# Performance work log

Measured on AMD Instinct MI355X. Metric: run time of the kernel, lower is better.

Reference implementation:

```python
import jax, jax.numpy as jnp
import numpy as np

B, L, D, V, S, R = 4096, 128, 100, 800000, 1024, 512
EPS = 1e-5

def setup_inputs() -> dict:
    key = jax.random.key(0)
    ks = jax.random.split(key, 10)
    bound = float(np.sqrt(6.0 / D))
    return {
        "statement_vecs": jax.random.normal(ks[0], (B, S), jnp.float32),
        "qa_ids": jax.random.randint(ks[1], (B, L, 2), 0, V),
        "qa_lens": jax.random.randint(ks[2], (B,), 0, L + 1),
        "emb": jax.random.uniform(ks[3], (V, D), jnp.float32, -bound, bound),
        "W1": jax.random.normal(ks[4], (2 * D + S, 2 * R), jnp.float32) * 0.02,
        "b1": jnp.zeros((2 * R,), jnp.float32),
        "g1": jnp.ones((2 * R,), jnp.float32),
        "beta1": jnp.zeros((2 * R,), jnp.float32),
        "W2": jax.random.normal(ks[5], (2 * R, R), jnp.float32) * 0.02,
        "b2": jnp.zeros((R,), jnp.float32),
        "g2": jnp.ones((R,), jnp.float32),
        "beta2": jnp.zeros((R,), jnp.float32),
        "W3": jax.random.normal(ks[6], (R, 1), jnp.float32) * 0.02,
        "b3": jnp.zeros((1,), jnp.float32),
    }

def _batchnorm(x, g, b):
    # BatchNorm1d in training mode: biased batch statistics over batch dim
    m = x.mean(0)
    v = ((x - m) ** 2).mean(0)
    return (x - m) * jax.lax.rsqrt(v + EPS) * g + b

def reference(statement_vecs, qa_ids, qa_lens, emb, W1, b1, g1, beta1, W2, b2, g2, beta2, W3, b3):
    # ragged mean-pool of (L_i, 2, D) concept embeddings, zero vector if length 0
    mask = (jnp.arange(L)[None, :] < qa_lens[:, None]).astype(emb.dtype)  # [B, L]
    qa_embed = emb[qa_ids]                                                # [B, L, 2, D]
    denom = jnp.maximum(qa_lens, 1).astype(emb.dtype)                     # avoid /0 (sum is 0 then)
    qa_pooled = (qa_embed * mask[:, :, None, None]).sum(1) / denom[:, None, None]  # [B, 2, D]
    qa_pooled = qa_pooled.reshape(B, 2 * D)
    qas = jnp.concatenate([qa_pooled, statement_vecs], axis=1)            # [B, 2D+S]
    # relation_extractor: Linear -> ReLU -> BN -> Linear -> BN -> ReLU
    h = _batchnorm(jax.nn.relu(qas @ W1 + b1), g1, beta1)
    h = jax.nn.relu(_batchnorm(h @ W2 + b2, g2, beta2))
    logits = h @ W3 + b3                                                  # [B, 1]
    return logits
```

## Files before the change

kernel.cpp:

```cpp
#include <hip/hip_runtime.h>
#include <hip/hip_bf16.h>

#define B_ 4096
#define L_ 128
#define D_ 100
#define S_ 1024
#define R_ 512
#define K1P_ 1280
#define N1_ 1024
#define EPS_ 1e-5f

typedef short bf16x8 __attribute__((ext_vector_type(8)));
typedef short short4v __attribute__((ext_vector_type(4)));
typedef float f32x4 __attribute__((ext_vector_type(4)));

static __device__ __forceinline__ short f2bf(float x) {
  union { float f; unsigned u; } c; c.f = x;
  unsigned r = (c.u + 0x7fffu + ((c.u >> 16) & 1u)) >> 16;
  return (short)r;
}
static __device__ __forceinline__ float bf2f(short x) {
  union { unsigned u; float f; } c; c.u = ((unsigned)(unsigned short)x) << 16;
  return c.f;
}

__global__ __launch_bounds__(256) void prep_kernel(
    const float* __restrict__ sv, const int* __restrict__ qa_ids,
    const int* __restrict__ qa_lens, const float* __restrict__ emb,
    const float* __restrict__ W1, short* __restrict__ qas,
    short* __restrict__ W1t) {
  int t = threadIdx.x;
  if (blockIdx.x < B_) {
    int b = blockIdx.x;
    __shared__ int ids[L_ * 2];
    __shared__ __align__(16) float partial[4][D_];
    int len = qa_lens[b];
    ids[t] = qa_ids[(size_t)b * (L_ * 2) + t];
    __syncthreads();
    int w = t >> 6, l = t & 63;
    if (l < 25) {
      float4 a = {0.f, 0.f, 0.f, 0.f};
      for (int r = w; r < 2 * len; r += 4) {
        const float* row = emb + (size_t)ids[r] * D_;
        float4 v = *reinterpret_cast<const float4*>(row + l * 4);
        a.x += v.x; a.y += v.y; a.z += v.z; a.w += v.w;
      }
      *reinterpret_cast<float4*>(&partial[w][l * 4]) = a;
    }
    __syncthreads();
    short* qrow = qas + (size_t)b * K1P_;
    if (t < 200) {
      int k = t / 100, d = t - k * 100;
      float s = partial[k][d] + partial[k + 2][d];
      qrow[t] = f2bf(s / (float)(len > 0 ? len : 1));
    }
    {
      float4 v = *reinterpret_cast<const float4*>(sv + (size_t)b * S_ + t * 4);
      short4v o;
      o[0] = f2bf(v.x); o[1] = f2bf(v.y); o[2] = f2bf(v.z); o[3] = f2bf(v.w);
      *(short4v*)&qrow[200 + t * 4] = o;
    }
    if (t < K1P_ - 1224) qrow[1224 + t] = 0;
  } else {
    __shared__ float tile[32][33];
    int bx = blockIdx.x - B_;
    int n0 = (bx & 31) * 32, k0 = (bx >> 5) * 32;
#pragma unroll
    for (int p = 0; p < 4; ++p) {
      int kk = (t >> 5) + p * 8, nn = t & 31;
      int k = k0 + kk;
      tile[kk][nn] = (k < 1224) ? W1[(size_t)k * N1_ + n0 + nn] : 0.f;
    }
    __syncthreads();
#pragma unroll
    for (int p = 0; p < 4; ++p) {
      int nn = (t >> 5) + p * 8, kk = t & 31;
      W1t[(size_t)(n0 + nn) * K1P_ + k0 + kk] = f2bf(tile[kk][nn]);
    }
  }
}

template <int ROWS>
static __device__ __forceinline__ void stage_tile64(
    const short* __restrict__ gp, int stride, int k0, short* lds, int t) {
#pragma unroll
  for (int p = 0; p < ROWS / 32; ++p) {
    int off16 = p * 256 + t;
    int r = off16 >> 3;
    int c = off16 & 7;
    int kc = c ^ (r & 7);
    const short* g = gp + (size_t)r * stride + k0 + kc * 8;
    __builtin_amdgcn_global_load_lds(
        (const __attribute__((address_space(1))) void*)g,
        (__attribute__((address_space(3))) void*)(lds + (size_t)off16 * 8),
        16, 0, 0);
  }
}

template <int BM, int BN, int WM, int WN, bool RELU, int NBIAS>
__global__ __launch_bounds__(256) void mfma_gemm(
    const short* __restrict__ A, const short* __restrict__ Bt,
    const float* __restrict__ biasp, short* __restrict__ C,
    float* __restrict__ part, int K, int N) {
  constexpr int FM = BM / WM / 16;
  constexpr int FN = BN / WN / 16;
  __shared__ short As[2][BM * 64];
  __shared__ short Bs[2][BN * 64];
  __shared__ float sred[WM][WN][FN][16];
  __shared__ float qred[WM][WN][FN][16];
  const int t = threadIdx.x;
  const int l = t & 63, w = t >> 6;
  const int wr = w / WN, wc = w % WN;
  const int row0 = blockIdx.y * BM, col0 = blockIdx.x * BN;
  const short* Ab = A + (size_t)row0 * K;
  const short* Bb = Bt + (size_t)col0 * K;
  f32x4 acc[FM][FN] = {};
  const int lrow = l & 15, lkc = l >> 4;
  const int nt = K / 64;
  stage_tile64<BM>(Ab, K, 0, As[0], t);
  stage_tile64<BN>(Bb, K, 0, Bs[0], t);
  __syncthreads();
  for (int ts = 0; ts < nt; ++ts) {
    const int cur = ts & 1;
    if (ts + 1 < nt) {
      stage_tile64<BM>(Ab, K, (ts + 1) * 64, As[cur ^ 1], t);
      stage_tile64<BN>(Bb, K, (ts + 1) * 64, Bs[cur ^ 1], t);
    }
    bf16x8 af[2][FM], bfr[2][FN];
#pragma unroll
    for (int ks = 0; ks < 2; ++ks) {
#pragma unroll
      for (int m = 0; m < FM; ++m) {
        int r = wr * (BM / WM) + m * 16 + lrow;
        int ch = (ks * 4 + lkc) ^ (r & 7);
        af[ks][m] = *(const bf16x8*)&As[cur][r * 64 + ch * 8];
      }
#pragma unroll
      for (int n = 0; n < FN; ++n) {
        int r = wc * (BN / WN) + n * 16 + lrow;
        int ch = (ks * 4 + lkc) ^ (r & 7);
        bfr[ks][n] = *(const bf16x8*)&Bs[cur][r * 64 + ch * 8];
      }
    }
#pragma unroll
    for (int ks = 0; ks < 2; ++ks)
#pragma unroll
      for (int m = 0; m < FM; ++m)
#pragma unroll
        for (int n = 0; n < FN; ++n)
          acc[m][n] = __builtin_amdgcn_mfma_f32_16x16x32_bf16(
              af[ks][m], bfr[ks][n], acc[m][n], 0, 0, 0);
    __syncthreads();
  }
  float ss[FN], qq[FN];
#pragma unroll
  for (int n = 0; n < FN; ++n) { ss[n] = 0.f; qq[n] = 0.f; }
#pragma unroll
  for (int m = 0; m < FM; ++m) {
#pragma unroll
    for (int n = 0; n < FN; ++n) {
      int col = col0 + wc * (BN / WN) + n * 16 + lrow;
      float bv = 0.f;
#pragma unroll
      for (int i = 0; i < NBIAS; ++i) bv += biasp[(size_t)i * N + col];
#pragma unroll
      for (int j = 0; j < 4; ++j) {
        int row = row0 + wr * (BM / WM) + m * 16 + (l >> 4) * 4 + j;
        float v = acc[m][n][j] + bv;
        if (RELU) v = fmaxf(v, 0.f);
        short vb = f2bf(v);
        C[(size_t)row * N + col] = vb;
        float f = bf2f(vb);
        ss[n] += f;
        qq[n] += f * f;
      }
    }
  }
#pragma unroll
  for (int n = 0; n < FN; ++n) {
    ss[n] += __shfl_xor(ss[n], 16);
    ss[n] += __shfl_xor(ss[n], 32);
    qq[n] += __shfl_xor(qq[n], 16);
    qq[n] += __shfl_xor(qq[n], 32);
  }
  if (l < 16) {
#pragma unroll
    for (int n = 0; n < FN; ++n) {
      sred[wr][wc][n][l] = ss[n];
      qred[wr][wc][n][l] = qq[n];
    }
  }
  __syncthreads();
  if (t < WN * FN * 16) {
    int c16 = t & 15, n = (t >> 4) % FN, wcc = t / (16 * FN);
    float s = 0.f, q = 0.f;
#pragma unroll
    for (int r = 0; r < WM; ++r) { s += sred[r][wcc][n][c16]; q += qred[r][wcc][n][c16]; }
    int col = col0 + wcc * (BN / WN) + n * 16 + c16;
    part[(size_t)blockIdx.y * 2 * N + col] = s;
    part[(size_t)blockIdx.y * 2 * N + N + col] = q;
  }
}

__global__ __launch_bounds__(256) void fold_tile(
    const float* __restrict__ part1, const float* __restrict__ W2,
    const float* __restrict__ b2, const float* __restrict__ g1,
    const float* __restrict__ beta1, short* __restrict__ W2pt,
    float* __restrict__ pbias) {
  int kt = blockIdx.x, jt = blockIdx.y;
  int t = threadIdx.x;
  int k0 = kt * 64, j0 = jt * 64;
  __shared__ float a1s[64], c1s[64];
  __shared__ float tT[64][65];
  __shared__ float bred[16][64];
  if (t < 64) {
    float s = 0.f, q = 0.f;
    for (int b = 0; b < 32; ++b) {
      s += part1[(size_t)b * 2048 + k0 + t];
      q += part1[(size_t)b * 2048 + 1024 + k0 + t];
    }
    float mean = s * (1.f / B_);
    float var = q * (1.f / B_) - mean * mean;
    float a = g1[k0 + t] * rsqrtf(var + EPS_);
    a1s[t] = a;
    c1s[t] = beta1[k0 + t] - mean * a;
  }
  __syncthreads();
  int g = t >> 4, j4 = t & 15;
  float pb0 = 0.f, pb1 = 0.f, pb2 = 0.f, pb3 = 0.f;
#pragma unroll
  for (int p = 0; p < 4; ++p) {
    int kk = g + p * 16;
    float4 wv = *(const float4*)&W2[(size_t)(k0 + kk) * R_ + j0 + j4 * 4];
    float a = a1s[kk], cc = c1s[kk];
    tT[j4 * 4 + 0][kk] = a * wv.x;
    tT[j4 * 4 + 1][kk] = a * wv.y;
    tT[j4 * 4 + 2][kk] = a * wv.z;
    tT[j4 * 4 + 3][kk] = a * wv.w;
    pb0 += cc * wv.x; pb1 += cc * wv.y; pb2 += cc * wv.z; pb3 += cc * wv.w;
  }
  bred[g][j4 * 4 + 0] = pb0;
  bred[g][j4 * 4 + 1] = pb1;
  bred[g][j4 * 4 + 2] = pb2;
  bred[g][j4 * 4 + 3] = pb3;
  __syncthreads();
#pragma unroll
  for (int p = 0; p < 4; ++p) {
    int jj = g + p * 16;
    short4v o;
    o[0] = f2bf(tT[jj][j4 * 4 + 0]);
    o[1] = f2bf(tT[jj][j4 * 4 + 1]);
    o[2] = f2bf(tT[jj][j4 * 4 + 2]);
    o[3] = f2bf(tT[jj][j4 * 4 + 3]);
    *(short4v*)&W2pt[(size_t)(j0 + jj) * N1_ + k0 + j4 * 4] = o;
  }
  if (t < 64) {
    float pbv = 0.f;
#pragma unroll
    for (int gg = 0; gg < 16; ++gg) pbv += bred[gg][t];
    if (kt == 0) pbv += b2[j0 + t];
    pbias[(size_t)kt * R_ + j0 + t] = pbv;
  }
}

__global__ __launch_bounds__(256) void reduce_bn2(
    const float* __restrict__ part2, const float* __restrict__ g2,
    const float* __restrict__ beta2, float* __restrict__ a2c2) {
  int j = blockIdx.x * 256 + threadIdx.x;
  if (j >= R_) return;
  float s = 0.f, q = 0.f;
  for (int b = 0; b < 64; ++b) {
    s += part2[(size_t)b * 1024 + j];
    q += part2[(size_t)b * 1024 + 512 + j];
  }
  float mean = s * (1.f / B_);
  float var = q * (1.f / B_) - mean * mean;
  float a = g2[j] * rsqrtf(var + EPS_);
  a2c2[j] = a;
  a2c2[R_ + j] = beta2[j] - mean * a;
}

__global__ __launch_bounds__(256) void final_kernel(
    const short* __restrict__ z2, const float* __restrict__ a2c2,
    const float* __restrict__ W3, const float* __restrict__ b3,
    float* __restrict__ out) {
  int wave = threadIdx.x >> 6;
  int lane = threadIdx.x & 63;
  int row = blockIdx.x * 4 + wave;
  const short* zr = z2 + (size_t)row * R_;
  int j0 = lane * 8;
  bf16x8 zv = *(const bf16x8*)&zr[j0];
  float acc = 0.f;
#pragma unroll
  for (int i = 0; i < 8; ++i) {
    float h = fmaxf(bf2f(zv[i]) * a2c2[j0 + i] + a2c2[R_ + j0 + i], 0.f);
    acc += h * W3[j0 + i];
  }
  for (int off = 32; off > 0; off >>= 1) acc += __shfl_down(acc, off, 64);
  if (lane == 0) out[row] = acc + b3[0];
}

extern "C" void kernel_launch(void* const* d_in, const int* in_sizes, int n_in,
                              void* d_out, int out_size, void* d_ws, size_t ws_size,
                              hipStream_t stream) {
  const float* sv      = (const float*)d_in[0];
  const int*   qa_ids  = (const int*)d_in[1];
  const int*   qa_lens = (const int*)d_in[2];
  const float* emb     = (const float*)d_in[3];
  const float* W1      = (const float*)d_in[4];
  const float* b1      = (const float*)d_in[5];
  const float* g1      = (const float*)d_in[6];
  const float* beta1   = (const float*)d_in[7];
  const float* W2      = (const float*)d_in[8];
  const float* b2      = (const float*)d_in[9];
  const float* g2      = (const float*)d_in[10];
  const float* beta2   = (const float*)d_in[11];
  const float* W3      = (const float*)d_in[12];
  const float* b3      = (const float*)d_in[13];
  float* out = (float*)d_out;

  char* p = (char*)d_ws;
  short* qas    = (short*)p; p += (size_t)B_ * K1P_ * 2;
  short* W1t    = (short*)p; p += (size_t)N1_ * K1P_ * 2;
  short* h1     = (short*)p; p += (size_t)B_ * N1_ * 2;
  short* W2pt   = (short*)p; p += (size_t)R_ * N1_ * 2;
  short* z2     = (short*)p; p += (size_t)B_ * R_ * 2;
  float* pbias  = (float*)p; p += (size_t)16 * R_ * 4;
  float* a2c2   = (float*)p; p += 2 * R_ * 4;
  float* part1  = (float*)p; p += (size_t)32 * 2 * N1_ * 4;
  float* part2  = (float*)p;

  prep_kernel<<<B_ + 32 * (K1P_ / 32), 256, 0, stream>>>(
      sv, qa_ids, qa_lens, emb, W1, qas, W1t);
  mfma_gemm<128, 64, 2, 2, true, 1>
      <<<dim3(N1_ / 64, B_ / 128), 256, 0, stream>>>(qas, W1t, b1, h1, part1, K1P_, N1_);
  fold_tile<<<dim3(16, 8), 256, 0, stream>>>(part1, W2, b2, g1, beta1, W2pt, pbias);
  mfma_gemm<64, 64, 2, 2, false, 16>
      <<<dim3(R_ / 64, B_ / 64), 256, 0, stream>>>(h1, W2pt, pbias, z2, part2, N1_, R_);
  reduce_bn2<<<2, 256, 0, stream>>>(part2, g2, beta2, a2c2);
  final_kernel<<<B_ / 4, 256, 0, stream>>>(z2, a2c2, W3, b3, out);
}
```

Baseline: 110.8 us.

## Split GEMM1 K-range and overlap statement GEMM with embedding pooling

```diff
diff --git a/kernel.cpp b/kernel.cpp
--- a/kernel.cpp
+++ b/kernel.cpp
@@ -6,7 +6,8 @@
 #define D_ 100
 #define S_ 1024
 #define R_ 512
-#define K1P_ 1280
+#define KP_ 256
+#define KS_ 1024
 #define N1_ 1024
 #define EPS_ 1e-5f
 
@@ -24,58 +25,187 @@
   return c.f;
 }
 
-__global__ __launch_bounds__(256) void prep_kernel(
+__global__ __launch_bounds__(256) void prep_w1(
+    const float* __restrict__ W1, short* __restrict__ W1t_p,
+    short* __restrict__ W1t_s) {
+  __shared__ float tile[32][33];
+  int bx = blockIdx.x;
+  int n0 = (bx & 31) * 32, k0 = (bx >> 5) * 32;
+  int t = threadIdx.x;
+#pragma unroll
+  for (int p = 0; p < 4; ++p) {
+    int kk = (t >> 5) + p * 8, nn = t & 31;
+    int k = k0 + kk;
+    tile[kk][nn] = (k < 1224) ? W1[(size_t)k * N1_ + n0 + nn] : 0.f;
+  }
+  __syncthreads();
+#pragma unroll
+  for (int p = 0; p < 4; ++p) {
+    int nn = (t >> 5) + p * 8, kk = t & 31;
+    int k = k0 + kk;
+    short val = f2bf(tile[kk][nn]);
+    if (k < 200)
+      W1t_p[(size_t)(n0 + nn) * KP_ + k] = val;
+    else if (k < 1224)
+      W1t_s[(size_t)(n0 + nn) * KS_ + (k - 200)] = val;
+  }
+  if ((bx >> 5) == 6) {
+    for (int i = t; i < 32 * 56; i += 256) {
+      int nn = i / 56, kk = i - nn * 56;
+      W1t_p[(size_t)(n0 + nn) * KP_ + 200 + kk] = 0;
+    }
+  }
+}
+
+__global__ __launch_bounds__(256) void pool_gemm1a(
     const float* __restrict__ sv, const int* __restrict__ qa_ids,
     const int* __restrict__ qa_lens, const float* __restrict__ emb,
-    const float* __restrict__ W1, short* __restrict__ qas,
-    short* __restrict__ W1t) {
+    const short* __restrict__ W1t_s, short* __restrict__ qas_p,
+    float* __restrict__ Cpart) {
+  __shared__ __align__(16) char smem[49152];
   int t = threadIdx.x;
   if (blockIdx.x < B_) {
     int b = blockIdx.x;
-    __shared__ int ids[L_ * 2];
-    __shared__ __align__(16) float partial[4][D_];
+    int* ids = (int*)smem;
+    float (*partial)[2][D_] = (float(*)[2][D_])(smem + 1024);
     int len = qa_lens[b];
     ids[t] = qa_ids[(size_t)b * (L_ * 2) + t];
     __syncthreads();
     int w = t >> 6, l = t & 63;
-    if (l < 25) {
-      float4 a = {0.f, 0.f, 0.f, 0.f};
-      for (int r = w; r < 2 * len; r += 4) {
+    int rs = l >> 5;
+    int li = l & 31;
+    if (li < 25) {
+      float4 a4[4];
+#pragma unroll
+      for (int q = 0; q < 4; ++q) a4[q] = {0.f, 0.f, 0.f, 0.f};
+      int n2 = 2 * len;
+      int r = 2 * w + rs;
+      for (; r + 24 < n2; r += 32) {
+#pragma unroll
+        for (int q = 0; q < 4; ++q) {
+          const float* row = emb + (size_t)ids[r + q * 8] * D_;
+          float4 v = *reinterpret_cast<const float4*>(row + li * 4);
+          a4[q].x += v.x; a4[q].y += v.y; a4[q].z += v.z; a4[q].w += v.w;
+        }
+      }
+      for (; r < n2; r += 8) {
         const float* row = emb + (size_t)ids[r] * D_;
-        float4 v = *reinterpret_cast<const float4*>(row + l * 4);
-        a.x += v.x; a.y += v.y; a.z += v.z; a.w += v.w;
-      }
-      *reinterpret_cast<float4*>(&partial[w][l * 4]) = a;
+        float4 v = *reinterpret_cast<const float4*>(row + li * 4);
+        a4[0].x += v.x; a4[0].y += v.y; a4[0].z += v.z; a4[0].w += v.w;
+      }
+      a4[0].x += a4[1].x + a4[2].x + a4[3].x;
+      a4[0].y += a4[1].y + a4[2].y + a4[3].y;
+      a4[0].z += a4[1].z + a4[2].z + a4[3].z;
+      a4[0].w += a4[1].w + a4[2].w + a4[3].w;
+      *reinterpret_cast<float4*>(&partial[w][rs][li * 4]) = a4[0];
     }
     __syncthreads();
-    short* qrow = qas + (size_t)b * K1P_;
+    short* qrow = qas_p + (size_t)b * KP_;
     if (t < 200) {
       int k = t / 100, d = t - k * 100;
-      float s = partial[k][d] + partial[k + 2][d];
+      float s = partial[0][k][d] + partial[1][k][d] +
+                partial[2][k][d] + partial[3][k][d];
       qrow[t] = f2bf(s / (float)(len > 0 ? len : 1));
-    }
-    {
-      float4 v = *reinterpret_cast<const float4*>(sv + (size_t)b * S_ + t * 4);
-      short4v o;
-      o[0] = f2bf(v.x); o[1] = f2bf(v.y); o[2] = f2bf(v.z); o[3] = f2bf(v.w);
-      *(short4v*)&qrow[200 + t * 4] = o;
-    }
-    if (t < K1P_ - 1224) qrow[1224 + t] = 0;
+    } else if (t < KP_) {
+      qrow[t] = 0;
+    }
   } else {
-    __shared__ float tile[32][33];
-    int bx = blockIdx.x - B_;
-    int n0 = (bx & 31) * 32, k0 = (bx >> 5) * 32;
-#pragma unroll
-    for (int p = 0; p < 4; ++p) {
-      int kk = (t >> 5) + p * 8, nn = t & 31;
-      int k = k0 + kk;
-      tile[kk][nn] = (k < 1224) ? W1[(size_t)k * N1_ + n0 + nn] : 0.f;
-    }
+    int bid = blockIdx.x - B_;
+    const int bx = bid & 15, by = bid >> 4;
+    short* As = (short*)smem;
+    short* Bs = (short*)(smem + 2 * 128 * 64 * 2);
+    const int l = t & 63, w = t >> 6;
+    const int wr = w >> 1, wc = w & 1;
+    const int row0 = by * 128, col0 = bx * 64;
+    const int lrow = l & 15, lkc = l >> 4;
+    f32x4 acc[4][2] = {};
+    float4 ra[4], rb[4];
+    auto loadA = [&](int k0) {
+#pragma unroll
+      for (int p = 0; p < 4; ++p) {
+        int idx = p * 256 + t;
+        int r = idx >> 3, c = idx & 7;
+        const float* g = sv + (size_t)(row0 + r) * KS_ + k0 + c * 8;
+        ra[p] = *reinterpret_cast<const float4*>(g);
+        rb[p] = *reinterpret_cast<const float4*>(g + 4);
+      }
+    };
+    auto writeA = [&](short* dst) {
+#pragma unroll
+      for (int p = 0; p < 4; ++p) {
+        int idx = p * 256 + t;
+        int r = idx >> 3, c = idx & 7;
+        int ch = c ^ (r & 7);
+        bf16x8 v;
+        v[0] = f2bf(ra[p].x); v[1] = f2bf(ra[p].y);
+        v[2] = f2bf(ra[p].z); v[3] = f2bf(ra[p].w);
+        v[4] = f2bf(rb[p].x); v[5] = f2bf(rb[p].y);
+        v[6] = f2bf(rb[p].z); v[7] = f2bf(rb[p].w);
+        *(bf16x8*)&dst[r * 64 + ch * 8] = v;
+      }
+    };
+    auto stageB = [&](int k0, short* dst) {
+#pragma unroll
+      for (int p = 0; p < 2; ++p) {
+        int idx = p * 256 + t;
+        int r = idx >> 3, c = idx & 7;
+        int kc = c ^ (r & 7);
+        const short* g = W1t_s + (size_t)(col0 + r) * KS_ + k0 + kc * 8;
+        __builtin_amdgcn_global_load_lds(
+            (const __attribute__((address_space(1))) void*)g,
+            (__attribute__((address_space(3))) void*)(dst + (size_t)idx * 8),
+            16, 0, 0);
+      }
+    };
+    loadA(0);
+    stageB(0, Bs);
+    writeA(As);
     __syncthreads();
-#pragma unroll
-    for (int p = 0; p < 4; ++p) {
-      int nn = (t >> 5) + p * 8, kk = t & 31;
-      W1t[(size_t)(n0 + nn) * K1P_ + k0 + kk] = f2bf(tile[kk][nn]);
+    const int nt = KS_ / 64;
+    for (int ts = 0; ts < nt; ++ts) {
+      const int cur = ts & 1;
+      if (ts + 1 < nt) {
+        loadA((ts + 1) * 64);
+        stageB((ts + 1) * 64, Bs + (cur ^ 1) * 64 * 64);
+      }
+      bf16x8 af[2][4], bfr[2][2];
+#pragma unroll
+      for (int ks = 0; ks < 2; ++ks) {
+#pragma unroll
+        for (int m = 0; m < 4; ++m) {
+          int r = wr * 64 + m * 16 + lrow;
+          int ch = (ks * 4 + lkc) ^ (r & 7);
+          af[ks][m] = *(const bf16x8*)&As[cur * 128 * 64 + r * 64 + ch * 8];
+        }
+#pragma unroll
+        for (int n = 0; n < 2; ++n) {
+          int r = wc * 32 + n * 16 + lrow;
+          int ch = (ks * 4 + lkc) ^ (r & 7);
+          bfr[ks][n] = *(const bf16x8*)&Bs[cur * 64 * 64 + r * 64 + ch * 8];
+        }
+      }
+#pragma unroll
+      for (int ks = 0; ks < 2; ++ks)
+#pragma unroll
+        for (int m = 0; m < 4; ++m)
+#pragma unroll
+          for (int n = 0; n < 2; ++n)
+            acc[m][n] = __builtin_amdgcn_mfma_f32_16x16x32_bf16(
+                af[ks][m], bfr[ks][n], acc[m][n], 0, 0, 0);
+      if (ts + 1 < nt) writeA(As + (cur ^ 1) * 128 * 64);
+      __syncthreads();
+    }
+#pragma unroll
+    for (int m = 0; m < 4; ++m) {
+#pragma unroll
+      for (int n = 0; n < 2; ++n) {
+        int col = col0 + wc * 32 + n * 16 + lrow;
+#pragma unroll
+        for (int j = 0; j < 4; ++j) {
+          int row = row0 + wr * 64 + m * 16 + (l >> 4) * 4 + j;
+          Cpart[(size_t)row * N1_ + col] = acc[m][n][j];
+        }
+      }
     }
   }
 }
@@ -97,11 +227,11 @@
   }
 }
 
-template <int BM, int BN, int WM, int WN, bool RELU, int NBIAS>
+template <int BM, int BN, int WM, int WN, bool RELU, int NBIAS, bool ADDC>
 __global__ __launch_bounds__(256) void mfma_gemm(
     const short* __restrict__ A, const short* __restrict__ Bt,
-    const float* __restrict__ biasp, short* __restrict__ C,
-    float* __restrict__ part, int K, int N) {
+    const float* __restrict__ biasp, const float* __restrict__ Cpart,
+    short* __restrict__ C, float* __restrict__ part, int K, int N) {
   constexpr int FM = BM / WM / 16;
   constexpr int FN = BN / WN / 16;
   __shared__ short As[2][BM * 64];
@@ -167,6 +297,7 @@
       for (int j = 0; j < 4; ++j) {
         int row = row0 + wr * (BM / WM) + m * 16 + (l >> 4) * 4 + j;
         float v = acc[m][n][j] + bv;
+        if constexpr (ADDC) v += Cpart[(size_t)row * N + col];
         if (RELU) v = fmaxf(v, 0.f);
         short vb = f2bf(v);
         C[(size_t)row * N + col] = vb;
@@ -320,8 +451,10 @@
   float* out = (float*)d_out;
 
   char* p = (char*)d_ws;
-  short* qas    = (short*)p; p += (size_t)B_ * K1P_ * 2;
-  short* W1t    = (short*)p; p += (size_t)N1_ * K1P_ * 2;
+  short* qas_p  = (short*)p; p += (size_t)B_ * KP_ * 2;
+  short* W1t_p  = (short*)p; p += (size_t)N1_ * KP_ * 2;
+  short* W1t_s  = (short*)p; p += (size_t)N1_ * KS_ * 2;
+  float* Cpart  = (float*)p; p += (size_t)B_ * N1_ * 4;
   short* h1     = (short*)p; p += (size_t)B_ * N1_ * 2;
   short* W2pt   = (short*)p; p += (size_t)R_ * N1_ * 2;
   short* z2     = (short*)p; p += (size_t)B_ * R_ * 2;
@@ -330,13 +463,13 @@
   float* part1  = (float*)p; p += (size_t)32 * 2 * N1_ * 4;
   float* part2  = (float*)p;
 
-  prep_kernel<<<B_ + 32 * (K1P_ / 32), 256, 0, stream>>>(
-      sv, qa_ids, qa_lens, emb, W1, qas, W1t);
-  mfma_gemm<128, 64, 2, 2, true, 1>
-      <<<dim3(N1_ / 64, B_ / 128), 256, 0, stream>>>(qas, W1t, b1, h1, part1, K1P_, N1_);
+  prep_w1<<<1280, 256, 0, stream>>>(W1, W1t_p, W1t_s);
+  pool_gemm1a<<<B_ + 512, 256, 0, stream>>>(sv, qa_ids, qa_lens, emb, W1t_s, qas_p, Cpart);
+  mfma_gemm<128, 64, 2, 2, true, 1, true>
+      <<<dim3(N1_ / 64, B_ / 128), 256, 0, stream>>>(qas_p, W1t_p, b1, Cpart, h1, part1, KP_, N1_);
   fold_tile<<<dim3(16, 8), 256, 0, stream>>>(part1, W2, b2, g1, beta1, W2pt, pbias);
-  mfma_gemm<64, 64, 2, 2, false, 16>
-      <<<dim3(R_ / 64, B_ / 64), 256, 0, stream>>>(h1, W2pt, pbias, z2, part2, N1_, R_);
+  mfma_gemm<64, 64, 2, 2, false, 16, false>
+      <<<dim3(R_ / 64, B_ / 64), 256, 0, stream>>>(h1, W2pt, pbias, nullptr, z2, part2, N1_, R_);
   reduce_bn2<<<2, 256, 0, stream>>>(part2, g2, beta2, a2c2);
   final_kernel<<<B_ / 4, 256, 0, stream>>>(z2, a2c2, W3, b3, out);
 }
```

Result: slower. 116.3 us (+5.0%).
